# Kernel tuning notes

Hardware: AMD Instinct MI355X
Metric: run time of the kernel (lower is better)

## Reference

```python
import jax, jax.numpy as jnp
import numpy as np

B, T, C = 2, 4096, 1024
NH, HS, BD, DELTA = 16, 64, 16, 32  # n_head, head_size, bond_dim, horizon window


def setup_inputs() -> dict:
    key = jax.random.key(0)
    ks = jax.random.split(key, 10)
    s = lambda k, shape: jax.random.normal(k, shape, jnp.float32) * 0.02
    return {
        "x": jax.random.normal(ks[0], (B, T, C), jnp.float32),
        "W_disp": s(ks[1], (C, NH * BD)),          # W_disp (no bias)
        "W_val": s(ks[2], (C, C)),                  # W_val (no bias)
        "rel_pos_emb": s(ks[3], (DELTA, BD)),       # rel pos embedding table
        "W_pos": s(ks[4], (BD, BD)),                # pos_proj (no bias)
        "W_sf": s(ks[5], (BD, 2 * BD)),             # strain_fused weight
        "b_sf": jnp.zeros((2 * BD,), jnp.float32),  # strain_fused bias
        "w_bond": s(ks[6], (BD,)),                  # bond_out (no bias)
        "w_dmg": s(ks[7], (BD,)),                   # damage_out weight
        "b_dmg": jnp.full((), -3.0, jnp.float32),   # damage_out bias init -3.0
        "W_cproj": s(ks[8], (C, C)),                # c_proj (no bias)
    }


def reference(x, W_disp, W_val, rel_pos_emb, W_pos, W_sf, b_sf, w_bond, w_dmg, b_dmg, W_cproj):
    Bb, Tt, Cc = x.shape
    delta = DELTA
    gelu = lambda v: jax.nn.gelu(v, approximate=False)

    # projections -> (B, nh, T, *)
    disp = (x @ W_disp).reshape(Bb, Tt, NH, BD).transpose(0, 2, 1, 3)
    val = (x @ W_val).reshape(Bb, Tt, NH, HS).transpose(0, 2, 1, 3)

    idx = jnp.arange(Tt)[:, None] + jnp.arange(delta)[None, :]  # (T, delta) into padded axis
    dpad = jnp.pad(disp, ((0, 0), (0, 0), (delta - 1, 0), (0, 0)))
    win = dpad[:, :, idx, :]                      # (B, nh, T, delta, bd)
    strain = win - disp[:, :, :, None, :]

    pos_feat = rel_pos_emb @ W_pos                # (delta, bd)
    fused = strain @ W_sf + b_sf                  # (B, nh, T, delta, 2bd)
    bf, df = fused[..., :BD], fused[..., BD:]
    bond_logits = gelu(bf + pos_feat) @ w_bond    # (B, nh, T, delta)
    damage = jax.nn.sigmoid(gelu(df) @ w_dmg + b_dmg)
    scores = bond_logits - damage * 10.0

    # causal/left-edge mask: kv_pos = t - delta + 1 + j >= 0
    cmask = (jnp.arange(Tt)[:, None] - delta + 1 + jnp.arange(delta)[None, :]) >= 0
    scores = jnp.where(cmask, scores, -jnp.inf)
    weights = jax.nn.softmax(scores, axis=-1)     # (B, nh, T, delta)

    vpad = jnp.pad(val, ((0, 0), (0, 0), (delta - 1, 0), (0, 0)))
    vw = vpad[:, :, idx, :]                       # (B, nh, T, delta, hs)
    out = jnp.einsum('bntj,bntjh->bnth', weights, vw)
    out = out.transpose(0, 2, 1, 3).reshape(Bb, Tt, Cc)
    return out @ W_cproj                          # resid dropout is eval no-op
```

## Files before the change

### kernel.cpp

```cpp
#include <hip/hip_runtime.h>
#include <hip/hip_bf16.h>

#define BB 2
#define TT 4096
#define CC 1024
#define NH 16
#define HS 64
#define BD 16
#define DELTA 32

typedef unsigned short u16;
typedef unsigned int u32;
typedef __bf16 bf16x8 __attribute__((ext_vector_type(8)));
typedef float floatx4 __attribute__((ext_vector_type(4)));

__device__ __forceinline__ float bf2f(u16 u) {
    unsigned v = ((unsigned)u) << 16;
    return __builtin_bit_cast(float, v);
}
__device__ __forceinline__ u16 f2bf(float x) {
    unsigned u = __builtin_bit_cast(unsigned, x);
    unsigned r = u + 0x7fffu + ((u >> 16) & 1u);
    return (u16)(r >> 16);
}
__device__ __forceinline__ float rcpf(float x) {
    float r;
    asm("v_rcp_f32 %0, %1" : "=v"(r) : "v"(x));
    return r;
}

__device__ __forceinline__ void storeC(float* p, float v) { *p = v; }
__device__ __forceinline__ void storeC(u16* p, float v) { *p = f2bf(v); }

#define GC0 0.3989422804014327f
#define GC1 (-0.06649038006690546f)
#define GC2 0.009973557010035818f
__device__ __forceinline__ float gelup(float x) {
    float u = x * x;
    float p = fmaf(u, fmaf(u, GC2, GC1), GC0);
    return x * fmaf(x, p, 0.5f);
}

__device__ __forceinline__ void load16_lds(const u16* g, u16* l) {
    __builtin_amdgcn_global_load_lds(
        (const __attribute__((address_space(1))) void*)g,
        (__attribute__((address_space(3))) void*)l, 16, 0, 0);
}

#define PREP_CONV   2048
#define PREP_WCAT   (PREP_CONV + 512)
#define PREP_POSF   (PREP_WCAT + 1)
#define PREP_T1     (PREP_POSF + 1024)
#define PREP_TOTAL  (PREP_T1 + 1024)

__global__ __launch_bounds__(256) void fused_prep(
    const float* __restrict__ x,     u16* __restrict__ xbf,
    const float* __restrict__ Wdisp, const float* __restrict__ Wsf,
    const float* __restrict__ rel,   const float* __restrict__ Wpos,
    u16* __restrict__ WcatT,         float* __restrict__ posf,
    const float* __restrict__ Wval,  const float* __restrict__ Wcproj,
    u16* __restrict__ WcpT)
{
    __shared__ u16 tile[32][33];
    const int bi  = blockIdx.x;
    const int tid = threadIdx.x;

    if (bi < PREP_CONV) {
        const long n4 = (long)BB * TT * CC / 4;
        long base = (long)bi * 256 + tid;
        #pragma unroll
        for (int i = 0; i < 4; ++i) {
            long idx = base + (long)i * (PREP_CONV * 256);
            if (idx < n4) {
                float4 v = ((const float4*)x)[idx];
                ushort4 o;
                o.x = f2bf(v.x); o.y = f2bf(v.y); o.z = f2bf(v.z); o.w = f2bf(v.w);
                ((ushort4*)xbf)[idx] = o;
            }
        }
    } else if (bi < PREP_WCAT) {
        const int r = bi - PREP_CONV;
        const int n = r >> 5, o = r & 31;
        float wcol[16];
        #pragma unroll
        for (int d = 0; d < 16; ++d) wcol[d] = Wsf[d * 32 + o];
        for (int c = tid; c < CC; c += 256) {
            float acc = 0.f;
            #pragma unroll
            for (int d = 0; d < 16; ++d)
                acc += Wdisp[c * (NH * BD) + n * 16 + d] * wcol[d];
            WcatT[(long)r * CC + c] = f2bf(acc);
        }
    } else if (bi < PREP_POSF) {
        for (int e = tid; e < DELTA * BD; e += 256) {
            int j = e >> 4, o2 = e & 15;
            float acc = 0.f;
            #pragma unroll
            for (int d = 0; d < 16; ++d)
                acc += rel[j * 16 + d] * Wpos[d * 16 + o2];
            posf[e] = acc;
        }
    } else {
        const bool isV = (bi < PREP_T1);
        const int t = bi - (isV ? PREP_POSF : PREP_T1);
        const float* in = isV ? Wval : Wcproj;
        u16* out = isV ? (WcatT + (size_t)512 * CC) : WcpT;
        const int bx = t & 31, by = t >> 5;
        const int tx = tid & 31, ty = tid >> 5;
        const int xcol = bx * 32 + tx;
        #pragma unroll
        for (int i = 0; i < 4; ++i) {
            int y = by * 32 + ty + i * 8;
            tile[ty + i * 8][tx] = f2bf(in[(long)y * CC + xcol]);
        }
        __syncthreads();
        const int x2 = by * 32 + tx;
        #pragma unroll
        for (int i = 0; i < 4; ++i) {
            int y2 = bx * 32 + ty + i * 8;
            out[(long)y2 * CC + x2] = tile[tx][ty + i * 8];
        }
    }
}

template <typename OUT_T>
__global__ __launch_bounds__(512, 4) void gemm_bt(
    const u16* __restrict__ A, const u16* __restrict__ Bt,
    OUT_T* __restrict__ C, int M, int N, int K)
{
    __shared__ __align__(16) u16 sA[128 * 64];
    __shared__ __align__(16) u16 sB[128 * 64];

    const int tid  = threadIdx.x;
    const int lane = tid & 63;
    const int wave = tid >> 6;
    const int wr = wave & 3;
    const int wc = wave >> 2;
    const int fr = lane & 15;
    const int q4 = lane >> 4;

    const u32 lin   = blockIdx.y * gridDim.x + blockIdx.x;
    const u32 total = gridDim.x * gridDim.y;
    const u32 qch   = total >> 3;
    const u32 nl    = (lin & 7) * qch + (lin >> 3);
    const int bx    = nl % gridDim.x;
    const int by    = nl / gridDim.x;
    const int m0 = by * 128;
    const int n0 = bx * 128;

    const int sg = tid & 7;
    const int sr = tid >> 3;

    floatx4 acc[2][4] = {};

    for (int k0 = 0; k0 < K; k0 += 64) {
        __syncthreads();
        #pragma unroll
        for (int rnd = 0; rnd < 2; ++rnd) {
            const int r = sr + rnd * 64;
            const int gsw = sg ^ (r & 7);
            load16_lds(A  + (long)(m0 + r) * K + k0 + gsw * 8,
                       &sA[rnd * 4096 + wave * 512]);
            load16_lds(Bt + (long)(n0 + r) * K + k0 + gsw * 8,
                       &sB[rnd * 4096 + wave * 512]);
        }
        __syncthreads();

        #pragma unroll
        for (int kh = 0; kh < 2; ++kh) {
            bf16x8 aF[2], bF[4];
            #pragma unroll
            for (int mt = 0; mt < 2; ++mt) {
                const int rr = wr * 32 + mt * 16 + fr;
                const int g = (kh * 4 + q4) ^ (rr & 7);
                aF[mt] = *(const bf16x8*)&sA[rr * 64 + g * 8];
            }
            #pragma unroll
            for (int nt = 0; nt < 4; ++nt) {
                const int rr = wc * 64 + nt * 16 + fr;
                const int g = (kh * 4 + q4) ^ (rr & 7);
                bF[nt] = *(const bf16x8*)&sB[rr * 64 + g * 8];
            }
            #pragma unroll
            for (int mt = 0; mt < 2; ++mt)
                #pragma unroll
                for (int nt = 0; nt < 4; ++nt)
                    acc[mt][nt] = __builtin_amdgcn_mfma_f32_16x16x32_bf16(
                        aF[mt], bF[nt], acc[mt][nt], 0, 0, 0);
        }
    }

    const int rbase = q4 << 2;
    #pragma unroll
    for (int mt = 0; mt < 2; ++mt)
        #pragma unroll
        for (int nt = 0; nt < 4; ++nt)
            #pragma unroll
            for (int r = 0; r < 4; ++r) {
                int m  = m0 + wr * 32 + mt * 16 + rbase + r;
                int nn = n0 + wc * 64 + nt * 16 + fr;
                storeC(C + (long)m * N + nn, acc[mt][nt][r]);
            }
}

__global__ __launch_bounds__(512) void attn_kernel(
    const u16* __restrict__ xcat,
    const float* __restrict__ posf,
    const float* __restrict__ b_sf, const float* __restrict__ w_bond,
    const float* __restrict__ w_dmg, const float* __restrict__ b_dmg,
    u16* __restrict__ att)
{
    __shared__ __align__(16) float sGs[95][36];
    __shared__ __align__(16) float sBias[32][36];
    __shared__ __align__(16) u16 sVT[64 * 128];
    __shared__ __align__(16) u16 sWb[64 * 128];
    __shared__ __align__(16) float sWBv[16], sWDv[16];

    const int tid = threadIdx.x;
    const int t_local = tid >> 5;
    const int j = tid & 31;
    const int t0 = blockIdx.x * 64;
    const int n = blockIdx.y;
    const int b = blockIdx.z;
    const long bT = (long)b * TT;

    const u32* xc = (const u32*)xcat;

    for (int e = tid; e < 95 * 16; e += 512) {
        int r = e >> 4, c = e & 15;
        int tok = t0 - 31 + r;
        u32 w = (tok >= 0) ? xc[(bT + tok) * 768 + n * 16 + c] : 0u;
        float2 f2 = make_float2(bf2f((u16)(w & 0xffffu)), bf2f((u16)(w >> 16)));
        *(float2*)&sGs[r][2 * c] = f2;
    }
    u32* sVT32 = (u32*)sVT;
    for (int e = tid; e < 48 * 32; e += 512) {
        int c = e & 31, rp = e >> 5;
        int tok0 = t0 - 31 + 2 * rp, tok1 = tok0 + 1;
        u32 a  = (tok0 >= 0 && tok0 < TT) ? xc[(bT + tok0) * 768 + 256 + n * 32 + c] : 0u;
        u32 bb = (tok1 >= 0 && tok1 < TT) ? xc[(bT + tok1) * 768 + 256 + n * 32 + c] : 0u;
        u32 lo = (a & 0xffffu) | (bb << 16);
        u32 hi = (a >> 16) | (bb & 0xffff0000u);
        int h0 = 2 * c, h1 = 2 * c + 1;
        int gr = rp >> 2, wq = rp & 3;
        int wd0 = wq | (((gr ^ (h0 & 7)) & 15) << 2);
        int wd1 = wq | (((gr ^ (h1 & 7)) & 15) << 2);
        sVT32[h0 * 64 + wd0] = lo;
        sVT32[h1 * 64 + wd1] = hi;
    }
    u32* sWb32 = (u32*)sWb;
    for (int e = tid; e < 64 * 64; e += 512) sWb32[e] = 0u;
    for (int e = tid; e < 1024; e += 512) {
        int jj = e >> 5, o = e & 31;
        sBias[jj][o] = b_sf[o] + ((o < 16) ? posf[jj * 16 + o] : 0.f);
    }
    if (tid < 16)      sWBv[tid]      = w_bond[tid];
    else if (tid < 32) sWDv[tid - 16] = w_dmg[tid - 16];
    __syncthreads();

    const float bdmg = b_dmg[0];
    float4 bb4[8];
    #pragma unroll
    for (int q = 0; q < 8; ++q) bb4[q] = *(const float4*)&sBias[j][4 * q];

    #pragma unroll
    for (int th = 0; th < 4; ++th) {
        const int tl = t_local + 16 * th;
        const float* Sp = sGs[tl + j];
        const float* Tp = sGs[tl + 31];
        const bool valid = (t0 + tl + j) >= 31;

        float bond = 0.f, dmg = 0.f;
        #pragma unroll
        for (int q = 0; q < 4; ++q) {
            float4 s = *(const float4*)&Sp[4 * q];
            float4 t = *(const float4*)&Tp[4 * q];
            float4 w = *(const float4*)&sWBv[4 * q];
            float4 bbv = bb4[q];
            bond += gelup(s.x - t.x + bbv.x) * w.x;
            bond += gelup(s.y - t.y + bbv.y) * w.y;
            bond += gelup(s.z - t.z + bbv.z) * w.z;
            bond += gelup(s.w - t.w + bbv.w) * w.w;
        }
        #pragma unroll
        for (int q = 0; q < 4; ++q) {
            float4 s = *(const float4*)&Sp[16 + 4 * q];
            float4 t = *(const float4*)&Tp[16 + 4 * q];
            float4 w = *(const float4*)&sWDv[4 * q];
            float4 bbv = bb4[4 + q];
            dmg += gelup(s.x - t.x + bbv.x) * w.x;
            dmg += gelup(s.y - t.y + bbv.y) * w.y;
            dmg += gelup(s.z - t.z + bbv.z) * w.z;
            dmg += gelup(s.w - t.w + bbv.w) * w.w;
        }
        float damage = rcpf(1.f + __expf(-(dmg + bdmg)));
        float score = bond - 10.f * damage;
        float p = valid ? __expf(score) : 0.f;
        float sum = p;
        #pragma unroll
        for (int off = 16; off; off >>= 1) sum += __shfl_xor(sum, off, 32);
        const int k = tl + j;
        const int slot = (k >> 3) ^ (tl & 7);
        sWb[tl * 128 + slot * 8 + (k & 7)] = f2bf(p * rcpf(sum));
    }
    __syncthreads();

    const int wave = tid >> 6;
    const int lane = tid & 63;
    const int ttile = wave & 3;
    const int htile = wave >> 2;
    const int fr = lane & 15;
    const int q4 = lane >> 4;
    const int r = ttile * 16 + fr;

    floatx4 o4[2] = {{0.f, 0.f, 0.f, 0.f}, {0.f, 0.f, 0.f, 0.f}};
    #pragma unroll
    for (int ks = 0; ks < 3; ++ks) {
        const int ga = (ks * 4 + q4) ^ (r & 7);
        bf16x8 aF = *(const bf16x8*)&sWb[r * 128 + ga * 8];
        #pragma unroll
        for (int ht = 0; ht < 2; ++ht) {
            const int h = htile * 32 + ht * 16 + fr;
            const int gb = (ks * 4 + q4) ^ (h & 7);
            bf16x8 bF = *(const bf16x8*)&sVT[h * 128 + gb * 8];
            o4[ht] = __builtin_amdgcn_mfma_f32_16x16x32_bf16(aF, bF, o4[ht], 0, 0, 0);
        }
    }
    const int trow = ttile * 16 + (q4 << 2);
    #pragma unroll
    for (int ht = 0; ht < 2; ++ht) {
        const int col = n * 64 + htile * 32 + ht * 16 + fr;
        #pragma unroll
        for (int rr = 0; rr < 4; ++rr)
            att[(bT + t0 + trow + rr) * 1024 + col] = f2bf(o4[ht][rr]);
    }
}

extern "C" void kernel_launch(void* const* d_in, const int* in_sizes, int n_in,
                              void* d_out, int out_size, void* d_ws, size_t ws_size,
                              hipStream_t stream)
{
    const float* x      = (const float*)d_in[0];
    const float* Wdisp  = (const float*)d_in[1];
    const float* Wval   = (const float*)d_in[2];
    const float* rel    = (const float*)d_in[3];
    const float* Wpos   = (const float*)d_in[4];
    const float* Wsf    = (const float*)d_in[5];
    const float* bsf    = (const float*)d_in[6];
    const float* wbond  = (const float*)d_in[7];
    const float* wdmg   = (const float*)d_in[8];
    const float* bdmg   = (const float*)d_in[9];
    const float* Wcproj = (const float*)d_in[10];

    char* ws = (char*)d_ws;
    const size_t O_WCAT = 0;
    const size_t O_WCPT = (size_t)4 << 20;
    const size_t O_POSF = (size_t)6 << 20;
    const size_t O_XBF  = (size_t)8 << 20;
    const size_t O_XCAT = (size_t)24 << 20;
    const size_t O_ATT  = (size_t)48 << 20;

    u16*   WcatT = (u16*)(ws + O_WCAT);
    u16*   WcpT  = (u16*)(ws + O_WCPT);
    float* posf  = (float*)(ws + O_POSF);
    u16*   xbf   = (u16*)(ws + O_XBF);
    u16*   xcat  = (u16*)(ws + O_XCAT);
    u16*   att   = (u16*)(ws + O_ATT);

    const int M = BB * TT;

    fused_prep<<<PREP_TOTAL, 256, 0, stream>>>(
        x, xbf, Wdisp, Wsf, rel, Wpos, WcatT, posf, Wval, Wcproj, WcpT);

    gemm_bt<u16><<<dim3(1536 / 128, M / 128), 512, 0, stream>>>(xbf, WcatT, xcat, M, 1536, CC);
    attn_kernel<<<dim3(TT / 64, NH, BB), 512, 0, stream>>>(xcat, posf, bsf, wbond, wdmg, bdmg, att);
    gemm_bt<float><<<dim3(1024 / 128, M / 128), 512, 0, stream>>>(att, WcpT, (float*)d_out, M, 1024, CC);
}
```

Baseline: 200.9 us.

## Add 256-thread 4x4-fragment GEMM for input projection and interleave attention gelu loops

Adds a 256-thread GEMM variant in which each of four waves computes a 64x64 output sub-tile with 4x4 MFMA fragments. Fragments loaded from shared memory are reused across more MFMAs, and this kernel replaces the 512-thread version for the fused disp/val projection. The attention kernel's bond/damage loops are also reordered so the four time rows are processed together, which shares weight and bias loads and exposes more independent work. The new GEMM uses more accumulator registers per thread and puts fewer waves in each block, which may reduce occupancy.

```diff
diff --git a/kernel.cpp b/kernel.cpp
--- a/kernel.cpp
+++ b/kernel.cpp
@@ -124,7 +124,85 @@
 }
 
 template <typename OUT_T>
-__global__ __launch_bounds__(512, 4) void gemm_bt(
+__global__ __launch_bounds__(256) void gemm_bt256(
+    const u16* __restrict__ A, const u16* __restrict__ Bt,
+    OUT_T* __restrict__ C, int M, int N, int K)
+{
+    __shared__ __align__(16) u16 sA[128 * 64];
+    __shared__ __align__(16) u16 sB[128 * 64];
+
+    const int tid  = threadIdx.x;
+    const int lane = tid & 63;
+    const int wave = tid >> 6;
+    const int wr = wave >> 1, wc = wave & 1;
+
+    const u32 lin   = blockIdx.y * gridDim.x + blockIdx.x;
+    const u32 total = gridDim.x * gridDim.y;
+    const u32 qch   = total >> 3;
+    const u32 nl    = (lin & 7) * qch + (lin >> 3);
+    const int bx    = nl % gridDim.x;
+    const int by    = nl / gridDim.x;
+    const int m0 = by * 128;
+    const int n0 = bx * 128;
+
+    const int sg = tid & 7;
+    const int sr = tid >> 3;
+
+    floatx4 acc[4][4] = {};
+
+    for (int k0 = 0; k0 < K; k0 += 64) {
+        __syncthreads();
+        #pragma unroll
+        for (int rnd = 0; rnd < 4; ++rnd) {
+            const int r = sr + rnd * 32;
+            const int gsw = sg ^ (r & 7);
+            load16_lds(A  + (long)(m0 + r) * K + k0 + gsw * 8,
+                       &sA[rnd * 2048 + wave * 512]);
+            load16_lds(Bt + (long)(n0 + r) * K + k0 + gsw * 8,
+                       &sB[rnd * 2048 + wave * 512]);
+        }
+        __syncthreads();
+
+        #pragma unroll
+        for (int kh = 0; kh < 2; ++kh) {
+            bf16x8 aF[4], bF[4];
+            #pragma unroll
+            for (int mt = 0; mt < 4; ++mt) {
+                const int rr = wr * 64 + mt * 16 + (lane & 15);
+                const int g = (kh * 4 + (lane >> 4)) ^ (rr & 7);
+                aF[mt] = *(const bf16x8*)&sA[rr * 64 + g * 8];
+            }
+            #pragma unroll
+            for (int nt = 0; nt < 4; ++nt) {
+                const int rr = wc * 64 + nt * 16 + (lane & 15);
+                const int g = (kh * 4 + (lane >> 4)) ^ (rr & 7);
+                bF[nt] = *(const bf16x8*)&sB[rr * 64 + g * 8];
+            }
+            #pragma unroll
+            for (int mt = 0; mt < 4; ++mt)
+                #pragma unroll
+                for (int nt = 0; nt < 4; ++nt)
+                    acc[mt][nt] = __builtin_amdgcn_mfma_f32_16x16x32_bf16(
+                        aF[mt], bF[nt], acc[mt][nt], 0, 0, 0);
+        }
+    }
+
+    const int rbase = (lane >> 4) << 2;
+    const int ccol  = lane & 15;
+    #pragma unroll
+    for (int mt = 0; mt < 4; ++mt)
+        #pragma unroll
+        for (int nt = 0; nt < 4; ++nt)
+            #pragma unroll
+            for (int r = 0; r < 4; ++r) {
+                int m  = m0 + wr * 64 + mt * 16 + rbase + r;
+                int nn = n0 + wc * 64 + nt * 16 + ccol;
+                storeC(C + (long)m * N + nn, acc[mt][nt][r]);
+            }
+}
+
+template <typename OUT_T>
+__global__ __launch_bounds__(512, 4) void gemm_bt512(
     const u16* __restrict__ A, const u16* __restrict__ Bt,
     OUT_T* __restrict__ C, int M, int N, int K)
 {
@@ -263,38 +341,52 @@
     #pragma unroll
     for (int q = 0; q < 8; ++q) bb4[q] = *(const float4*)&sBias[j][4 * q];
 
+    const float* Sp[4];
+    const float* Tp[4];
+    #pragma unroll
+    for (int th = 0; th < 4; ++th) {
+        Sp[th] = sGs[t_local + 16 * th + j];
+        Tp[th] = sGs[t_local + 16 * th + 31];
+    }
+
+    float bond[4] = {0.f, 0.f, 0.f, 0.f};
+    float dmg[4]  = {0.f, 0.f, 0.f, 0.f};
+
+    #pragma unroll
+    for (int q = 0; q < 4; ++q) {
+        float4 w   = *(const float4*)&sWBv[4 * q];
+        float4 bbv = bb4[q];
+        #pragma unroll
+        for (int th = 0; th < 4; ++th) {
+            float4 s = *(const float4*)&Sp[th][4 * q];
+            float4 t = *(const float4*)&Tp[th][4 * q];
+            bond[th] += gelup(s.x - t.x + bbv.x) * w.x;
+            bond[th] += gelup(s.y - t.y + bbv.y) * w.y;
+            bond[th] += gelup(s.z - t.z + bbv.z) * w.z;
+            bond[th] += gelup(s.w - t.w + bbv.w) * w.w;
+        }
+    }
+    #pragma unroll
+    for (int q = 0; q < 4; ++q) {
+        float4 w   = *(const float4*)&sWDv[4 * q];
+        float4 bbv = bb4[4 + q];
+        #pragma unroll
+        for (int th = 0; th < 4; ++th) {
+            float4 s = *(const float4*)&Sp[th][16 + 4 * q];
+            float4 t = *(const float4*)&Tp[th][16 + 4 * q];
+            dmg[th] += gelup(s.x - t.x + bbv.x) * w.x;
+            dmg[th] += gelup(s.y - t.y + bbv.y) * w.y;
+            dmg[th] += gelup(s.z - t.z + bbv.z) * w.z;
+            dmg[th] += gelup(s.w - t.w + bbv.w) * w.w;
+        }
+    }
+
     #pragma unroll
     for (int th = 0; th < 4; ++th) {
         const int tl = t_local + 16 * th;
-        const float* Sp = sGs[tl + j];
-        const float* Tp = sGs[tl + 31];
         const bool valid = (t0 + tl + j) >= 31;
-
-        float bond = 0.f, dmg = 0.f;
-        #pragma unroll
-        for (int q = 0; q < 4; ++q) {
-            float4 s = *(const float4*)&Sp[4 * q];
-            float4 t = *(const float4*)&Tp[4 * q];
-            float4 w = *(const float4*)&sWBv[4 * q];
-            float4 bbv = bb4[q];
-            bond += gelup(s.x - t.x + bbv.x) * w.x;
-            bond += gelup(s.y - t.y + bbv.y) * w.y;
-            bond += gelup(s.z - t.z + bbv.z) * w.z;
-            bond += gelup(s.w - t.w + bbv.w) * w.w;
-        }
-        #pragma unroll
-        for (int q = 0; q < 4; ++q) {
-            float4 s = *(const float4*)&Sp[16 + 4 * q];
-            float4 t = *(const float4*)&Tp[16 + 4 * q];
-            float4 w = *(const float4*)&sWDv[4 * q];
-            float4 bbv = bb4[4 + q];
-            dmg += gelup(s.x - t.x + bbv.x) * w.x;
-            dmg += gelup(s.y - t.y + bbv.y) * w.y;
-            dmg += gelup(s.z - t.z + bbv.z) * w.z;
-            dmg += gelup(s.w - t.w + bbv.w) * w.w;
-        }
-        float damage = rcpf(1.f + __expf(-(dmg + bdmg)));
-        float score = bond - 10.f * damage;
+        float damage = rcpf(1.f + __expf(-(dmg[th] + bdmg)));
+        float score = bond[th] - 10.f * damage;
         float p = valid ? __expf(score) : 0.f;
         float sum = p;
         #pragma unroll
@@ -372,7 +464,7 @@
     fused_prep<<<PREP_TOTAL, 256, 0, stream>>>(
         x, xbf, Wdisp, Wsf, rel, Wpos, WcatT, posf, Wval, Wcproj, WcpT);
 
-    gemm_bt<u16><<<dim3(1536 / 128, M / 128), 512, 0, stream>>>(xbf, WcatT, xcat, M, 1536, CC);
+    gemm_bt256<u16><<<dim3(1536 / 128, M / 128), 256, 0, stream>>>(xbf, WcatT, xcat, M, 1536, CC);
     attn_kernel<<<dim3(TT / 64, NH, BB), 512, 0, stream>>>(xcat, posf, bsf, wbond, wdmg, bdmg, att);
-    gemm_bt<float><<<dim3(1024 / 128, M / 128), 512, 0, stream>>>(att, WcpT, (float*)d_out, M, 1024, CC);
-}
+    gemm_bt512<float><<<dim3(1024 / 128, M / 128), 512, 0, stream>>>(att, WcpT, (float*)d_out, M, 1024, CC);
+}
```

Result: no change. 198.7 us (-1.1%).
